# Optimization experiments

Hardware: AMD Instinct MI355X
Metric: run time of the kernel (lower is better)

## Reference

```python
import jax, jax.numpy as jnp
import numpy as np

EPS = 1e-5  # torch LayerNorm default

def _ln(x, g, b):
    m = jnp.mean(x, axis=-1, keepdims=True)
    v = jnp.mean((x - m) ** 2, axis=-1, keepdims=True)
    return (x - m) * jax.lax.rsqrt(v + EPS) * g + b

def setup_inputs() -> dict:
    key = jax.random.key(0)
    ks = jax.random.split(key, 12)
    N_sup = N_res = 768
    c_z = 128   # input_dim
    c = 128     # num_intermediate_channel
    c_out = 128 # output_dim
    s = 0.02
    d = {}
    d["act_s"] = jax.random.normal(ks[0], (N_sup, N_sup, c_z), jnp.float32)
    d["act_r"] = jax.random.normal(ks[1], (N_res, N_res, c_z), jnp.float32)
    d["mask_r"] = (jax.random.uniform(ks[2], (N_res, N_res)) > 0.1).astype(jnp.float32)
    # input LayerNorm params
    d["ln_in_g"] = jnp.ones((c_z,), jnp.float32)
    d["ln_in_b"] = jnp.zeros((c_z,), jnp.float32)
    # projections (stored as [in, out], y = x @ W + b)
    d["w_lp"] = (jax.random.normal(ks[3], (c_z, c)) * s).astype(jnp.float32)
    d["b_lp"] = jnp.zeros((c,), jnp.float32)
    d["w_rp"] = (jax.random.normal(ks[4], (c_z, c)) * s).astype(jnp.float32)
    d["b_rp"] = jnp.zeros((c,), jnp.float32)
    # gates (bias_init=1)
    d["w_lg"] = (jax.random.normal(ks[5], (c_z, c)) * s).astype(jnp.float32)
    d["b_lg"] = jnp.ones((c,), jnp.float32)
    d["w_rg"] = (jax.random.normal(ks[6], (c_z, c)) * s).astype(jnp.float32)
    d["b_rg"] = jnp.ones((c,), jnp.float32)
    # center LayerNorm
    d["ln_c_g"] = jnp.ones((c,), jnp.float32)
    d["ln_c_b"] = jnp.zeros((c,), jnp.float32)
    # output projection
    d["w_out"] = (jax.random.normal(ks[7], (c, c_out)) * s).astype(jnp.float32)
    d["b_out"] = jnp.zeros((c_out,), jnp.float32)
    return d

def reference(act_s, act_r, mask_r, ln_in_g, ln_in_b, w_lp, b_lp, w_rp, b_rp,
              w_lg, b_lg, w_rg, b_rg, ln_c_g, ln_c_b, w_out, b_out):
    m = mask_r[..., None]                                   # [N_res, N_res, 1]
    s = _ln(act_s, ln_in_g, ln_in_b)                        # [N_sup, N_sup, c_z]
    r = _ln(act_r, ln_in_g, ln_in_b)                        # [N_res, N_res, c_z]
    left = (s @ w_lp + b_lp) * jax.nn.sigmoid(s @ w_lg + b_lg)
    right = (m * (r @ w_rp + b_rp)) * jax.nn.sigmoid(r @ w_rg + b_rg)
    left_line = left.sum(axis=0)                            # [N_sup, c] (aggr_by_row)
    right_line = right.sum(axis=0)                          # [N_res, c]
    act = jnp.einsum('ik,jk->ijk', left_line, right_line)   # [N_sup, N_res, c]
    act = _ln(act, ln_c_g, ln_c_b)
    return act @ w_out + b_out                              # [N_sup, N_res, c_out]
```

## Files before the change

### kernel.cpp

```cpp
#include <hip/hip_runtime.h>
#include <math.h>

#define NRES 768
#define C    128
#define LNEPS 1e-5f
#define TA   16
#define ACH  48
#define MI   16
#define NIT  (NRES / MI)
#define XBUF (MI * 256)

typedef __attribute__((ext_vector_type(8))) short bf16x8;
typedef __attribute__((ext_vector_type(4))) float f32x4;

__device__ __forceinline__ uint32_t bf16rn(float f) {
    uint32_t u = __float_as_uint(f);
    return (u + 0x7FFFu + ((u >> 16) & 1u)) >> 16;
}

__device__ __forceinline__ void split2(float a, float b, uint32_t& hi, uint32_t& lo) {
    uint32_t ha = bf16rn(a), hb = bf16rn(b);
    float ra = a - __uint_as_float(ha << 16);
    float rb = b - __uint_as_float(hb << 16);
    hi = ha | (hb << 16);
    lo = bf16rn(ra) | (bf16rn(rb) << 16);
}

__device__ __forceinline__ void stage_row3(const float4& x, int row, int t,
                                           char* hiB, char* loB, char* sqB) {
    const int byte = (row * 256 + 8 * (t & 31)) ^ ((row & 15) << 4);
    uint2 uh, ul, uq;
    split2(x.x, x.y, uh.x, ul.x);
    split2(x.z, x.w, uh.y, ul.y);
    uq.x = bf16rn(x.x * x.x) | (bf16rn(x.y * x.y) << 16);
    uq.y = bf16rn(x.z * x.z) | (bf16rn(x.w * x.w) << 16);
    *(uint2*)(hiB + byte) = uh;
    *(uint2*)(loB + byte) = ul;
    *(uint2*)(sqB + byte) = uq;
}

template <int RIGHT>
__global__ __launch_bounds__(256, 3) void line_mfma(
    const float* __restrict__ act,
    const float* __restrict__ mask,
    const float* __restrict__ ln_g, const float* __restrict__ ln_b,
    const float* __restrict__ wP, const float* __restrict__ bP,
    const float* __restrict__ wG, const float* __restrict__ bG,
    float* __restrict__ part)
{
    __shared__ char  sHi[XBUF];
    __shared__ char  sLo[XBUF];
    __shared__ char  sSq[XBUF];
    __shared__ float sM[TA * MI];

    const int t = threadIdx.x;
    const int w = t >> 6;
    const int l = t & 63;
    const int i0  = (blockIdx.x % NIT) * MI;
    const int ach = blockIdx.x / NIT;
    const int a0  = ach * TA;

    bf16x8 bfr[4][4];
    float  sQ[4], cB[4];
#pragma unroll
    for (int nt = 0; nt < 4; ++nt) {
        const float* wsrc = (nt < 2) ? wP : wG;
        const int n = w * 32 + (nt & 1) * 16 + (l & 15);
        float sacc = 0.f, tacc = 0.f;
#pragma unroll
        for (int kk = 0; kk < 4; ++kk) {
            bf16x8 f;
#pragma unroll
            for (int jj = 0; jj < 8; ++jj) {
                const int k = kk * 32 + (l >> 4) * 8 + jj;
                const float wv = wsrc[k * C + n];
                const uint32_t q = bf16rn(ln_g[k] * wv);
                f[jj] = (short)q;
                sacc += __uint_as_float(q << 16);
                tacc += ln_b[k] * wv;
            }
            bfr[nt][kk] = f;
        }
        sacc += __shfl_xor(sacc, 16); sacc += __shfl_xor(sacc, 32);
        tacc += __shfl_xor(tacc, 16); tacc += __shfl_xor(tacc, 32);
        sQ[nt] = sacc;
        cB[nt] = tacc + ((nt < 2) ? bP[n] : bG[n]);
    }

    bf16x8 onesf;
#pragma unroll
    for (int jj = 0; jj < 8; ++jj) onesf[jj] = (short)0x3F80;

    if (RIGHT) {
        sM[t] = mask[(size_t)(a0 + (t >> 4)) * NRES + i0 + (t & 15)];
    }

    float lacc[2][4];
#pragma unroll
    for (int ntp = 0; ntp < 2; ++ntp)
#pragma unroll
        for (int jr = 0; jr < 4; ++jr) lacc[ntp][jr] = 0.f;

    const float* srcbase = act + (size_t)a0 * (NRES * C) + (size_t)i0 * C;

    float4 xv[2], xn[2];
#pragma unroll
    for (int j = 0; j < 2; ++j)
        xv[j] = *(const float4*)(srcbase + 4 * (t + 256 * j));

    for (int al = 0; al < TA; ++al) {
        if (al + 1 < TA) {
            const float* srcn = srcbase + (size_t)(al + 1) * (NRES * C);
#pragma unroll
            for (int j = 0; j < 2; ++j)
                xn[j] = *(const float4*)(srcn + 4 * (t + 256 * j));
        }

#pragma unroll
        for (int j = 0; j < 2; ++j)
            stage_row3(xv[j], (t >> 5) + 8 * j, t, sHi, sLo, sSq);
        __syncthreads();

        const f32x4 zero = {0.f, 0.f, 0.f, 0.f};
        f32x4 acc[4], accS = zero, accS2 = zero;
#pragma unroll
        for (int nt = 0; nt < 4; ++nt) acc[nt] = zero;

#pragma unroll
        for (int kk = 0; kk < 4; ++kk) {
            const int row  = l & 15;
            const int byte = (row * 256 + (kk * 32 + (l >> 4) * 8) * 2) ^ ((row & 15) << 4);
            const bf16x8 ah  = *(const bf16x8*)(sHi + byte);
            const bf16x8 alo = *(const bf16x8*)(sLo + byte);
            const bf16x8 asq = *(const bf16x8*)(sSq + byte);
            acc[0] = __builtin_amdgcn_mfma_f32_16x16x32_bf16(ah,  bfr[0][kk], acc[0], 0, 0, 0);
            acc[0] = __builtin_amdgcn_mfma_f32_16x16x32_bf16(alo, bfr[0][kk], acc[0], 0, 0, 0);
            acc[1] = __builtin_amdgcn_mfma_f32_16x16x32_bf16(ah,  bfr[1][kk], acc[1], 0, 0, 0);
            acc[1] = __builtin_amdgcn_mfma_f32_16x16x32_bf16(alo, bfr[1][kk], acc[1], 0, 0, 0);
            acc[2] = __builtin_amdgcn_mfma_f32_16x16x32_bf16(ah,  bfr[2][kk], acc[2], 0, 0, 0);
            acc[3] = __builtin_amdgcn_mfma_f32_16x16x32_bf16(ah,  bfr[3][kk], acc[3], 0, 0, 0);
            accS  = __builtin_amdgcn_mfma_f32_16x16x32_bf16(ah,  onesf, accS,  0, 0, 0);
            accS2 = __builtin_amdgcn_mfma_f32_16x16x32_bf16(asq, onesf, accS2, 0, 0, 0);
        }

        float mk[4] = {1.f, 1.f, 1.f, 1.f};
        if (RIGHT) {
            const float4 m4 = *(const float4*)&sM[al * MI + (l >> 4) * 4];
            mk[0] = m4.x; mk[1] = m4.y; mk[2] = m4.z; mk[3] = m4.w;
        }
#pragma unroll
        for (int jr = 0; jr < 4; ++jr) {
            const float m_  = accS[jr] * (1.f / C);
            const float var = accS2[jr] * (1.f / C) - m_ * m_;
            const float inv = rsqrtf(var + LNEPS);
#pragma unroll
            for (int ntp = 0; ntp < 2; ++ntp) {
                const float P = (acc[ntp][jr]     - m_ * sQ[ntp])     * inv + cB[ntp];
                const float G = (acc[ntp + 2][jr] - m_ * sQ[ntp + 2]) * inv + cB[ntp + 2];
                const float sg = __builtin_amdgcn_rcpf(1.f + __expf(-G));
                lacc[ntp][jr] += P * sg * mk[jr];
            }
        }
        __syncthreads();

        xv[0] = xn[0]; xv[1] = xn[1];
    }

    float* dst = part + (size_t)ach * (NRES * C);
#pragma unroll
    for (int ntp = 0; ntp < 2; ++ntp)
#pragma unroll
        for (int jr = 0; jr < 4; ++jr)
            dst[(size_t)(i0 + (l >> 4) * 4 + jr) * C +
                w * 32 + ntp * 16 + (l & 15)] = lacc[ntp][jr];
}

__global__ __launch_bounds__(256) void reduce_part(const float* __restrict__ part,
                                                   float* __restrict__ line) {
    const int idx = blockIdx.x * 256 + threadIdx.x;
    float s = 0.f;
#pragma unroll 8
    for (int p = 0; p < ACH; ++p) s += part[(size_t)p * (NRES * C) + idx];
    line[idx] = s;
}

__global__ __launch_bounds__(256, 3) void out_mfma(
    const float* __restrict__ lline,
    const float* __restrict__ rline,
    const float* __restrict__ cg, const float* __restrict__ cb,
    const float* __restrict__ wO, const float* __restrict__ bO,
    float* __restrict__ out)
{
    __shared__ char sHi[64 * 256];
    __shared__ char sLo[64 * 256];
    __shared__ char sSq[64 * 256];

    const int t = threadIdx.x;
    const int w = t >> 6;
    const int l = t & 63;
    const int i  = blockIdx.x / 12;
    const int j0 = (blockIdx.x % 12) * 64;

    bf16x8 bfr[2][4];
    float  sQ[2], cB[2];
#pragma unroll
    for (int nt = 0; nt < 2; ++nt) {
        const int n = w * 32 + nt * 16 + (l & 15);
        float sacc = 0.f, tacc = 0.f;
#pragma unroll
        for (int kk = 0; kk < 4; ++kk) {
            bf16x8 f;
#pragma unroll
            for (int jj = 0; jj < 8; ++jj) {
                const int k = kk * 32 + (l >> 4) * 8 + jj;
                const float wv = wO[k * C + n];
                const uint32_t q = bf16rn(cg[k] * wv);
                f[jj] = (short)q;
                sacc += __uint_as_float(q << 16);
                tacc += cb[k] * wv;
            }
            bfr[nt][kk] = f;
        }
        sacc += __shfl_xor(sacc, 16); sacc += __shfl_xor(sacc, 32);
        tacc += __shfl_xor(tacc, 16); tacc += __shfl_xor(tacc, 32);
        sQ[nt] = sacc;
        cB[nt] = tacc + bO[n];
    }

    bf16x8 onesf;
#pragma unroll
    for (int jj = 0; jj < 8; ++jj) onesf[jj] = (short)0x3F80;

    const int c4 = 4 * (t & 31);
    const float4 l4 = *(const float4*)(lline + (size_t)i * C + c4);

    const float* rsrc = rline + (size_t)j0 * C;
#pragma unroll
    for (int j = 0; j < 8; ++j) {
        const float4 r = *(const float4*)(rsrc + 4 * (t + 256 * j));
        float4 p;
        p.x = l4.x * r.x; p.y = l4.y * r.y; p.z = l4.z * r.z; p.w = l4.w * r.w;
        stage_row3(p, (t >> 5) + 8 * j, t, sHi, sLo, sSq);
    }
    __syncthreads();

    const f32x4 zero = {0.f, 0.f, 0.f, 0.f};
#pragma unroll
    for (int mt = 0; mt < 4; ++mt) {
        f32x4 acc[2], accS = zero, accS2 = zero;
#pragma unroll
        for (int nt = 0; nt < 2; ++nt) acc[nt] = zero;
#pragma unroll
        for (int kk = 0; kk < 4; ++kk) {
            const int row  = mt * 16 + (l & 15);
            const int byte = (row * 256 + (kk * 32 + (l >> 4) * 8) * 2) ^ ((row & 15) << 4);
            const bf16x8 ah  = *(const bf16x8*)(sHi + byte);
            const bf16x8 alo = *(const bf16x8*)(sLo + byte);
            const bf16x8 asq = *(const bf16x8*)(sSq + byte);
            acc[0] = __builtin_amdgcn_mfma_f32_16x16x32_bf16(ah,  bfr[0][kk], acc[0], 0, 0, 0);
            acc[0] = __builtin_amdgcn_mfma_f32_16x16x32_bf16(alo, bfr[0][kk], acc[0], 0, 0, 0);
            acc[1] = __builtin_amdgcn_mfma_f32_16x16x32_bf16(ah,  bfr[1][kk], acc[1], 0, 0, 0);
            acc[1] = __builtin_amdgcn_mfma_f32_16x16x32_bf16(alo, bfr[1][kk], acc[1], 0, 0, 0);
            accS  = __builtin_amdgcn_mfma_f32_16x16x32_bf16(ah,  onesf, accS,  0, 0, 0);
            accS2 = __builtin_amdgcn_mfma_f32_16x16x32_bf16(asq, onesf, accS2, 0, 0, 0);
        }
#pragma unroll
        for (int jr = 0; jr < 4; ++jr) {
            const float m_  = accS[jr] * (1.f / C);
            const float var = accS2[jr] * (1.f / C) - m_ * m_;
            const float inv = rsqrtf(var + LNEPS);
#pragma unroll
            for (int nt = 0; nt < 2; ++nt)
                out[((size_t)i * NRES + j0 + mt * 16 + (l >> 4) * 4 + jr) * C +
                    w * 32 + nt * 16 + (l & 15)] =
                    (acc[nt][jr] - m_ * sQ[nt]) * inv + cB[nt];
        }
    }
}

extern "C" void kernel_launch(void* const* d_in, const int* in_sizes, int n_in,
                              void* d_out, int out_size, void* d_ws, size_t ws_size,
                              hipStream_t stream) {
    const float* act_s = (const float*)d_in[0];
    const float* act_r = (const float*)d_in[1];
    const float* mask  = (const float*)d_in[2];
    const float* ln_g  = (const float*)d_in[3];
    const float* ln_b  = (const float*)d_in[4];
    const float* w_lp  = (const float*)d_in[5];
    const float* b_lp  = (const float*)d_in[6];
    const float* w_rp  = (const float*)d_in[7];
    const float* b_rp  = (const float*)d_in[8];
    const float* w_lg  = (const float*)d_in[9];
    const float* b_lg  = (const float*)d_in[10];
    const float* w_rg  = (const float*)d_in[11];
    const float* b_rg  = (const float*)d_in[12];
    const float* ln_cg = (const float*)d_in[13];
    const float* ln_cb = (const float*)d_in[14];
    const float* w_out = (const float*)d_in[15];
    const float* b_out = (const float*)d_in[16];
    float* out = (float*)d_out;

    float* part       = (float*)d_ws;
    float* left_line  = part + (size_t)ACH * NRES * C;
    float* right_line = left_line + NRES * C;

    line_mfma<0><<<ACH * NIT, 256, 0, stream>>>(act_s, nullptr, ln_g, ln_b,
                                                w_lp, b_lp, w_lg, b_lg, part);
    reduce_part<<<NRES * C / 256, 256, 0, stream>>>(part, left_line);
    line_mfma<1><<<ACH * NIT, 256, 0, stream>>>(act_r, mask, ln_g, ln_b,
                                                w_rp, b_rp, w_rg, b_rg, part);
    reduce_part<<<NRES * C / 256, 256, 0, stream>>>(part, right_line);
    out_mfma<<<NRES * 12, 256, 0, stream>>>(left_line, right_line, ln_cg, ln_cb,
                                            w_out, b_out, out);
}
```

Before: 366.4 us.

## Double-buffer LDS staging in line kernel to drop one barrier per row

Moves the three bf16 staging buffers (hi, lo, square) to a two-slot ping-pong scheme. The next row is staged into the idle slot after the current row's MFMA and epilogue, and the global prefetch now runs two rows ahead. This leaves one __syncthreads per iteration instead of two and lets the staging writes overlap other waves' compute. In exchange LDS use doubles to about 24KB per block, which may lower occupancy at 3 blocks per CU, and holding fragments for all four K slices raises register pressure.

```diff
diff --git a/kernel.cpp b/kernel.cpp
--- a/kernel.cpp
+++ b/kernel.cpp
@@ -48,9 +48,9 @@
     const float* __restrict__ wG, const float* __restrict__ bG,
     float* __restrict__ part)
 {
-    __shared__ char  sHi[XBUF];
-    __shared__ char  sLo[XBUF];
-    __shared__ char  sSq[XBUF];
+    __shared__ char  sHi[2][XBUF];
+    __shared__ char  sLo[2][XBUF];
+    __shared__ char  sSq[2][XBUF];
     __shared__ float sM[TA * MI];
 
     const int t = threadIdx.x;
@@ -103,23 +103,36 @@
 
     const float* srcbase = act + (size_t)a0 * (NRES * C) + (size_t)i0 * C;
 
-    float4 xv[2], xn[2];
+    float4 xn[2];
+    {
+        float4 x0[2];
+#pragma unroll
+        for (int j = 0; j < 2; ++j)
+            x0[j] = *(const float4*)(srcbase + 4 * (t + 256 * j));
+#pragma unroll
+        for (int j = 0; j < 2; ++j)
+            stage_row3(x0[j], (t >> 5) + 8 * j, t, sHi[0], sLo[0], sSq[0]);
+    }
 #pragma unroll
     for (int j = 0; j < 2; ++j)
-        xv[j] = *(const float4*)(srcbase + 4 * (t + 256 * j));
-
+        xn[j] = *(const float4*)(srcbase + (size_t)(NRES * C) + 4 * (t + 256 * j));
+    __syncthreads();
+
+    int cur = 0;
     for (int al = 0; al < TA; ++al) {
-        if (al + 1 < TA) {
-            const float* srcn = srcbase + (size_t)(al + 1) * (NRES * C);
-#pragma unroll
-            for (int j = 0; j < 2; ++j)
-                xn[j] = *(const float4*)(srcn + 4 * (t + 256 * j));
-        }
-
-#pragma unroll
-        for (int j = 0; j < 2; ++j)
-            stage_row3(xv[j], (t >> 5) + 8 * j, t, sHi, sLo, sSq);
-        __syncthreads();
+        const char* hiB = sHi[cur];
+        const char* loB = sLo[cur];
+        const char* sqB = sSq[cur];
+
+        bf16x8 fh[4], fl[4], fq[4];
+#pragma unroll
+        for (int kk = 0; kk < 4; ++kk) {
+            const int row  = l & 15;
+            const int byte = (row * 256 + (kk * 32 + (l >> 4) * 8) * 2) ^ ((row & 15) << 4);
+            fh[kk] = *(const bf16x8*)(hiB + byte);
+            fl[kk] = *(const bf16x8*)(loB + byte);
+            fq[kk] = *(const bf16x8*)(sqB + byte);
+        }
 
         const f32x4 zero = {0.f, 0.f, 0.f, 0.f};
         f32x4 acc[4], accS = zero, accS2 = zero;
@@ -128,19 +141,14 @@
 
 #pragma unroll
         for (int kk = 0; kk < 4; ++kk) {
-            const int row  = l & 15;
-            const int byte = (row * 256 + (kk * 32 + (l >> 4) * 8) * 2) ^ ((row & 15) << 4);
-            const bf16x8 ah  = *(const bf16x8*)(sHi + byte);
-            const bf16x8 alo = *(const bf16x8*)(sLo + byte);
-            const bf16x8 asq = *(const bf16x8*)(sSq + byte);
-            acc[0] = __builtin_amdgcn_mfma_f32_16x16x32_bf16(ah,  bfr[0][kk], acc[0], 0, 0, 0);
-            acc[0] = __builtin_amdgcn_mfma_f32_16x16x32_bf16(alo, bfr[0][kk], acc[0], 0, 0, 0);
-            acc[1] = __builtin_amdgcn_mfma_f32_16x16x32_bf16(ah,  bfr[1][kk], acc[1], 0, 0, 0);
-            acc[1] = __builtin_amdgcn_mfma_f32_16x16x32_bf16(alo, bfr[1][kk], acc[1], 0, 0, 0);
-            acc[2] = __builtin_amdgcn_mfma_f32_16x16x32_bf16(ah,  bfr[2][kk], acc[2], 0, 0, 0);
-            acc[3] = __builtin_amdgcn_mfma_f32_16x16x32_bf16(ah,  bfr[3][kk], acc[3], 0, 0, 0);
-            accS  = __builtin_amdgcn_mfma_f32_16x16x32_bf16(ah,  onesf, accS,  0, 0, 0);
-            accS2 = __builtin_amdgcn_mfma_f32_16x16x32_bf16(asq, onesf, accS2, 0, 0, 0);
+            acc[0] = __builtin_amdgcn_mfma_f32_16x16x32_bf16(fh[kk], bfr[0][kk], acc[0], 0, 0, 0);
+            acc[0] = __builtin_amdgcn_mfma_f32_16x16x32_bf16(fl[kk], bfr[0][kk], acc[0], 0, 0, 0);
+            acc[1] = __builtin_amdgcn_mfma_f32_16x16x32_bf16(fh[kk], bfr[1][kk], acc[1], 0, 0, 0);
+            acc[1] = __builtin_amdgcn_mfma_f32_16x16x32_bf16(fl[kk], bfr[1][kk], acc[1], 0, 0, 0);
+            acc[2] = __builtin_amdgcn_mfma_f32_16x16x32_bf16(fh[kk], bfr[2][kk], acc[2], 0, 0, 0);
+            acc[3] = __builtin_amdgcn_mfma_f32_16x16x32_bf16(fh[kk], bfr[3][kk], acc[3], 0, 0, 0);
+            accS   = __builtin_amdgcn_mfma_f32_16x16x32_bf16(fh[kk], onesf, accS,  0, 0, 0);
+            accS2  = __builtin_amdgcn_mfma_f32_16x16x32_bf16(fq[kk], onesf, accS2, 0, 0, 0);
         }
 
         float mk[4] = {1.f, 1.f, 1.f, 1.f};
@@ -161,9 +169,21 @@
                 lacc[ntp][jr] += P * sg * mk[jr];
             }
         }
+
+        if (al + 1 < TA) {
+#pragma unroll
+            for (int j = 0; j < 2; ++j)
+                stage_row3(xn[j], (t >> 5) + 8 * j, t,
+                           (char*)sHi[cur ^ 1], (char*)sLo[cur ^ 1], (char*)sSq[cur ^ 1]);
+            if (al + 2 < TA) {
+                const float* srcn = srcbase + (size_t)(al + 2) * (NRES * C);
+#pragma unroll
+                for (int j = 0; j < 2; ++j)
+                    xn[j] = *(const float4*)(srcn + 4 * (t + 256 * j));
+            }
+        }
         __syncthreads();
-
-        xv[0] = xn[0]; xv[1] = xn[1];
+        cur ^= 1;
     }
 
     float* dst = part + (size_t)ach * (NRES * C);
```

After: 380.3 us. +3.8%, slower.
